# Kernel optimization log

Hardware: AMD Instinct MI355X
Metric: run time of the kernel (lower is better)

Reference implementation:

```python
import jax, jax.numpy as jnp
import numpy as np

H, C = 8, 32          # heads, per-head channels (h_feats)
NEG_SLOPE = 0.2


def setup_inputs() -> dict:
    key = jax.random.key(0)
    ks = jax.random.split(key, 9)
    N, E, F_IN, F_E = 50000, 800000, 128, 16
    x = jax.random.normal(ks[0], (N, F_IN), jnp.float32)
    edge_index = jax.random.randint(ks[1], (2, E), 0, N, jnp.int64)
    edge_attr = jax.random.normal(ks[2], (E, F_E), jnp.float32)
    s = 1.0 / np.sqrt(F_IN)
    W = jax.random.normal(ks[3], (H * C, F_IN), jnp.float32) * s
    W_edge = jax.random.normal(ks[4], (H * C, F_E), jnp.float32) * (1.0 / np.sqrt(F_E))
    att_src = jax.random.normal(ks[5], (H, C), jnp.float32) * (1.0 / np.sqrt(C))
    att_dst = jax.random.normal(ks[6], (H, C), jnp.float32) * (1.0 / np.sqrt(C))
    att_edge = jax.random.normal(ks[7], (H, C), jnp.float32) * (1.0 / np.sqrt(C))
    bias = jnp.zeros((C,), jnp.float32)
    return {"x": x, "edge_index": edge_index, "edge_attr": edge_attr,
            "W": W, "W_edge": W_edge, "att_src": att_src, "att_dst": att_dst,
            "att_edge": att_edge, "bias": bias}


def reference(x, edge_index, edge_attr, W, W_edge, att_src, att_dst, att_edge, bias):
    N = x.shape[0]
    src, dst = edge_index[0], edge_index[1]

    # --- add self loops, edge_attr fill_value='mean' (per-dst mean of incoming attrs) ---
    deg = jax.ops.segment_sum(jnp.ones_like(dst, dtype=edge_attr.dtype), dst, num_segments=N)
    loop_attr = jax.ops.segment_sum(edge_attr, dst, num_segments=N) / jnp.maximum(deg, 1.0)[:, None]
    loop = jnp.arange(N, dtype=src.dtype)
    src = jnp.concatenate([src, loop])
    dst = jnp.concatenate([dst, loop])
    ea = jnp.concatenate([edge_attr, loop_attr], axis=0)  # [E+N, F_e]

    # --- node projection and per-node attention terms ---
    xh = (x @ W.T).reshape(N, H, C)                      # [N,H,C]
    a_src = jnp.einsum('nhc,hc->nh', xh, att_src)        # [N,H]
    a_dst = jnp.einsum('nhc,hc->nh', xh, att_dst)        # [N,H]

    # edge attention folded: (lin_edge(e).view(E,H,C) * att_edge).sum(-1) == e @ M
    M = jnp.einsum('hcf,hc->fh', W_edge.reshape(H, C, -1), att_edge)  # [F_e,H]
    a_edge = ea @ M                                      # [E+N,H]

    alpha = a_src[src] + a_dst[dst] + a_edge             # [E+N,H]
    alpha = jnp.where(alpha >= 0, alpha, NEG_SLOPE * alpha)

    # --- scatter-softmax over edges grouped by dst node ---
    amax = jax.ops.segment_max(alpha, dst, num_segments=N)  # every node has a self loop
    ex = jnp.exp(alpha - amax[dst])
    denom = jax.ops.segment_sum(ex, dst, num_segments=N)
    att = ex / denom[dst]                                # [E+N,H]

    # --- weighted message scatter-sum ---
    msg = xh[src] * att[..., None]                       # [E+N,H,C]
    out = jax.ops.segment_sum(msg, dst, num_segments=N)  # [N,H,C]
    return out.mean(axis=1) + bias                       # concat=False -> head mean
```

## Files before the change

kernel.cpp:

```cpp
#include <hip/hip_runtime.h>
#include <hip/hip_fp16.h>
#include <math.h>

#define H 8
#define C 32
#define HC 256
#define FE 16
#define FIN 128
#define NEG_SLOPE 0.2f

typedef __attribute__((ext_vector_type(8))) short bf16x8;
typedef __attribute__((ext_vector_type(4))) float f32x4;

__device__ __forceinline__ unsigned short f2bf(float f) {
  unsigned int u = __float_as_uint(f);
  unsigned int lsb = (u >> 16) & 1u;
  u += 0x7fffu + lsb;
  return (unsigned short)(u >> 16);
}
__device__ __forceinline__ float bf2f(unsigned short s) {
  return __uint_as_float(((unsigned int)s) << 16);
}
__device__ __forceinline__ unsigned short f2h(float f) {
  return __half_as_ushort(__float2half(f));
}
__device__ __forceinline__ float h2f(unsigned short s) {
  return __half2float(__ushort_as_half(s));
}

__device__ __forceinline__ void split8(const float* v, bf16x8& hi, bf16x8& lo) {
#pragma unroll
  for (int i = 0; i < 8; ++i) {
    unsigned int u = __float_as_uint(v[i]);
    unsigned int hu = u & 0xffff0000u;
    float r = v[i] - __uint_as_float(hu);
    hi[i] = (short)(hu >> 16);
    lo[i] = (short)f2bf(r);
  }
}

__global__ __launch_bounds__(256) void k_xh(const float* __restrict__ x,
                                            const unsigned short* __restrict__ Whi,
                                            const unsigned short* __restrict__ Wlo,
                                            const float* __restrict__ att_src,
                                            const float* __restrict__ att_dst,
                                            unsigned short* __restrict__ xhb,
                                            float* __restrict__ a_src,
                                            float* __restrict__ a_dst,
                                            unsigned short* __restrict__ a_srch, int N) {
  int t = threadIdx.x;
  int w = t >> 6, lane = t & 63;
  int n15 = lane & 15, q = lane >> 4;
  int nodeBase = blockIdx.x * 128 + w * 32;
  int chBase = blockIdx.y * 128;

  f32x4 acc[8][2];
#pragma unroll
  for (int mt = 0; mt < 8; ++mt)
#pragma unroll
    for (int nt = 0; nt < 2; ++nt) acc[mt][nt] = (f32x4)(0.f);

  for (int ks = 0; ks < 4; ++ks) {
    int kOff = ks * 32 + q * 8;
    bf16x8 Bhi[2], Blo[2];
#pragma unroll
    for (int nt = 0; nt < 2; ++nt) {
      int node = nodeBase + nt * 16 + n15;
      int rn = (node < N) ? node : (N - 1);
      const float* px = &x[(size_t)rn * FIN + kOff];
      float vb[8];
      *(float4*)&vb[0] = *(const float4*)px;
      *(float4*)&vb[4] = *(const float4*)(px + 4);
      split8(vb, Bhi[nt], Blo[nt]);
    }
#pragma unroll
    for (int mt = 0; mt < 8; ++mt) {
      int widx = ((chBase + mt * 16 + n15) << 7) + kOff;
      bf16x8 Ahi = *(const bf16x8*)&Whi[widx];
      bf16x8 Alo = *(const bf16x8*)&Wlo[widx];
#pragma unroll
      for (int nt = 0; nt < 2; ++nt) {
        acc[mt][nt] = __builtin_amdgcn_mfma_f32_16x16x32_bf16(Ahi, Bhi[nt], acc[mt][nt], 0, 0, 0);
        acc[mt][nt] = __builtin_amdgcn_mfma_f32_16x16x32_bf16(Ahi, Blo[nt], acc[mt][nt], 0, 0, 0);
        acc[mt][nt] = __builtin_amdgcn_mfma_f32_16x16x32_bf16(Alo, Bhi[nt], acc[mt][nt], 0, 0, 0);
      }
    }
  }

  float ps[2][4] = {{0.f,0.f,0.f,0.f},{0.f,0.f,0.f,0.f}};
  float pd[2][4] = {{0.f,0.f,0.f,0.f},{0.f,0.f,0.f,0.f}};
#pragma unroll
  for (int mt = 0; mt < 8; ++mt) {
    int hl = mt >> 1;
#pragma unroll
    for (int r = 0; r < 4; ++r) {
      int ch = chBase + mt * 16 + q * 4 + r;
      float as_c = att_src[ch], ad_c = att_dst[ch];
#pragma unroll
      for (int nt = 0; nt < 2; ++nt) {
        float val = acc[mt][nt][r];
        ps[nt][hl] = fmaf(val, as_c, ps[nt][hl]);
        pd[nt][hl] = fmaf(val, ad_c, pd[nt][hl]);
      }
    }
#pragma unroll
    for (int nt = 0; nt < 2; ++nt) {
      int node = nodeBase + nt * 16 + n15;
      if (node < N) {
        ushort4 us;
        us.x = f2bf(acc[mt][nt][0]); us.y = f2bf(acc[mt][nt][1]);
        us.z = f2bf(acc[mt][nt][2]); us.w = f2bf(acc[mt][nt][3]);
        *(ushort4*)&xhb[(size_t)node * HC + chBase + mt * 16 + q * 4] = us;
      }
    }
  }
#pragma unroll
  for (int nt = 0; nt < 2; ++nt)
#pragma unroll
    for (int hl = 0; hl < 4; ++hl) {
      ps[nt][hl] += __shfl_xor(ps[nt][hl], 16, 64);
      ps[nt][hl] += __shfl_xor(ps[nt][hl], 32, 64);
      pd[nt][hl] += __shfl_xor(pd[nt][hl], 16, 64);
      pd[nt][hl] += __shfl_xor(pd[nt][hl], 32, 64);
    }
  if (q == 0) {
#pragma unroll
    for (int nt = 0; nt < 2; ++nt) {
      int node = nodeBase + nt * 16 + n15;
      if (node < N) {
        *(float4*)&a_src[node * H + blockIdx.y * 4] = make_float4(ps[nt][0], ps[nt][1], ps[nt][2], ps[nt][3]);
        *(float4*)&a_dst[node * H + blockIdx.y * 4] = make_float4(pd[nt][0], pd[nt][1], pd[nt][2], pd[nt][3]);
        unsigned int p0 = (unsigned int)f2h(ps[nt][0]) | ((unsigned int)f2h(ps[nt][1]) << 16);
        unsigned int p1 = (unsigned int)f2h(ps[nt][2]) | ((unsigned int)f2h(ps[nt][3]) << 16);
        *(uint2*)&a_srch[(size_t)node * H + blockIdx.y * 4] = make_uint2(p0, p1);
      }
    }
  }
}

__global__ __launch_bounds__(256) void k_deg(const int* __restrict__ ei,
                                             int* __restrict__ deg,
                                             int* __restrict__ rank,
                                             const float* __restrict__ W,
                                             unsigned short* __restrict__ Whi,
                                             unsigned short* __restrict__ Wlo, int E) {
  int e = blockIdx.x * 256 + threadIdx.x;
  if (e < HC * FIN) {
    float v = W[e];
    unsigned int u = __float_as_uint(v);
    unsigned int hu = u & 0xffff0000u;
    Whi[e] = (unsigned short)(hu >> 16);
    Wlo[e] = f2bf(v - __uint_as_float(hu));
  }
  if (e < E) rank[e] = atomicAdd(&deg[ei[E + e]], 1);
}

__global__ __launch_bounds__(256) void k_scan1(const int* __restrict__ deg,
                                               int* __restrict__ bsum, int N) {
  int t = threadIdx.x;
  int i = blockIdx.x * 256 + t;
  int v = (i < N) ? deg[i] : 0;
#pragma unroll
  for (int m = 1; m < 64; m <<= 1) v += __shfl_xor(v, m, 64);
  __shared__ int wsum[4];
  if ((t & 63) == 0) wsum[t >> 6] = v;
  __syncthreads();
  if (t == 0) bsum[blockIdx.x] = wsum[0] + wsum[1] + wsum[2] + wsum[3];
}

__global__ __launch_bounds__(256) void k_scan23(const int* __restrict__ deg,
                                                const int* __restrict__ bsum,
                                                int* __restrict__ rowptr, int N, int E, int nb) {
  __shared__ int sb[256];
  __shared__ int buf[256];
  int t = threadIdx.x;
  sb[t] = (t < nb) ? bsum[t] : 0;
  int i = blockIdx.x * 256 + t;
  int v = (i < N) ? deg[i] : 0;
  buf[t] = v;
  __syncthreads();
  for (int off = 1; off < 256; off <<= 1) {
    int y1 = (t >= off) ? sb[t - off] : 0;
    int y2 = (t >= off) ? buf[t - off] : 0;
    __syncthreads();
    sb[t] += y1;
    buf[t] += y2;
    __syncthreads();
  }
  int bofs = (blockIdx.x == 0) ? 0 : sb[blockIdx.x - 1];
  if (i < N) rowptr[i] = bofs + buf[t] - v;
  if (i == 0) rowptr[N] = E;
}

__global__ __launch_bounds__(256) void k_edge_scatter(const int* __restrict__ ei,
                                                      const float* __restrict__ ea,
                                                      const float* __restrict__ W_edge,
                                                      const float* __restrict__ att_edge,
                                                      const unsigned short* __restrict__ a_srch,
                                                      const int* __restrict__ rowptr,
                                                      const int* __restrict__ rank,
                                                      unsigned int* __restrict__ recs,
                                                      int* __restrict__ sarr, int E) {
  __shared__ float Ms[FE * H];
  int t = threadIdx.x;
  if (t < FE * H) {
    int f = t >> 3, h = t & 7;
    float acc = 0.f;
#pragma unroll
    for (int c = 0; c < C; ++c)
      acc += W_edge[(h * C + c) * FE + f] * att_edge[h * C + c];
    Ms[f * H + h] = acc;
  }
  __syncthreads();
  int e0 = blockIdx.x * 512 + t;
  int e1 = e0 + 256;
  bool va = (e0 < E), vb = (e1 < E);
  int ca = va ? e0 : 0, cb = vb ? e1 : 0;
  int s0 = ei[ca], d0 = ei[E + ca];
  int s1 = ei[cb], d1 = ei[E + cb];
  const float4* pA = (const float4*)&ea[(size_t)ca * FE];
  const float4* pB = (const float4*)&ea[(size_t)cb * FE];
  float4 A0 = pA[0], A1 = pA[1], A2 = pA[2], A3 = pA[3];
  float4 B0 = pB[0], B1 = pB[1], B2 = pB[2], B3 = pB[3];
  int rk0 = rank[ca], rk1 = rank[cb];
  int rp0 = rowptr[d0], rp1 = rowptr[d1];
  uint4 asA = *(const uint4*)&a_srch[(size_t)s0 * H];
  uint4 asB = *(const uint4*)&a_srch[(size_t)s1 * H];

  float eavA[FE] = {A0.x, A0.y, A0.z, A0.w, A1.x, A1.y, A1.z, A1.w,
                    A2.x, A2.y, A2.z, A2.w, A3.x, A3.y, A3.z, A3.w};
  float eavB[FE] = {B0.x, B0.y, B0.z, B0.w, B1.x, B1.y, B1.z, B1.w,
                    B2.x, B2.y, B2.z, B2.w, B3.x, B3.y, B3.z, B3.w};
  float oA[H], oB[H];
#pragma unroll
  for (int h = 0; h < H; ++h) {
    float aa = 0.f, ab = 0.f;
#pragma unroll
    for (int f = 0; f < FE; ++f) {
      float m = Ms[f * H + h];
      aa += eavA[f] * m;
      ab += eavB[f] * m;
    }
    oA[h] = aa; oB[h] = ab;
  }
  unsigned int asw[2][4] = {{asA.x, asA.y, asA.z, asA.w}, {asB.x, asB.y, asB.z, asB.w}};
  if (va) {
    int pos = rp0 + rk0;
    unsigned int rec[H];
#pragma unroll
    for (int h = 0; h < H; ++h) {
      float asv = h2f((unsigned short)((h & 1) ? (asw[0][h >> 1] >> 16) : (asw[0][h >> 1] & 0xffffu)));
      rec[h] = (unsigned int)f2h(oA[h] + asv) | ((unsigned int)f2h(oA[h]) << 16);
    }
    uint4* rp = (uint4*)&recs[(size_t)pos * 8];
    rp[0] = make_uint4(rec[0], rec[1], rec[2], rec[3]);
    rp[1] = make_uint4(rec[4], rec[5], rec[6], rec[7]);
    sarr[pos] = s0;
  }
  if (vb) {
    int pos = rp1 + rk1;
    unsigned int rec[H];
#pragma unroll
    for (int h = 0; h < H; ++h) {
      float asv = h2f((unsigned short)((h & 1) ? (asw[1][h >> 1] >> 16) : (asw[1][h >> 1] & 0xffffu)));
      rec[h] = (unsigned int)f2h(oB[h] + asv) | ((unsigned int)f2h(oB[h]) << 16);
    }
    uint4* rp = (uint4*)&recs[(size_t)pos * 8];
    rp[0] = make_uint4(rec[0], rec[1], rec[2], rec[3]);
    rp[1] = make_uint4(rec[4], rec[5], rec[6], rec[7]);
    sarr[pos] = s1;
  }
}

__global__ __launch_bounds__(256) void k_node(const unsigned short* __restrict__ xhb,
                                              const float* __restrict__ a_src,
                                              const float* __restrict__ a_dst,
                                              const unsigned int* __restrict__ recs,
                                              const int* __restrict__ sarr,
                                              const int* __restrict__ rowptr,
                                              const float* __restrict__ bias,
                                              float* __restrict__ out, int N) {
  __shared__ float wlds[4][512];
  __shared__ int   slds[4][64];
  int wv = threadIdx.x >> 6;
  int lane = threadIdx.x & 63;
  int n = blockIdx.x * 4 + wv;
  if (n >= N) return;
  int start = rowptr[n];
  int deg = rowptr[n + 1] - start;
  int jmax = (deg < 64) ? deg : 64;
  int nit = (jmax + 7) >> 3;
  int padded = nit << 3;
  int h = lane & 7, esub = lane >> 3;
  float adst = a_dst[n * H + h];
  float asrc = a_src[n * H + h];

  if (lane < padded) slds[wv][lane] = (lane < jmax) ? sarr[start + lane] : n;

  const unsigned int* rb = recs + (size_t)start * 8 + lane;
  unsigned int u[8] = {0, 0, 0, 0, 0, 0, 0, 0};
#pragma unroll
  for (int it = 0; it < 8; ++it)
    if (it < nit) u[it] = rb[it * 64];

  float den = 0.f, psum = 0.f;
#pragma unroll
  for (int it = 0; it < 8; ++it)
    if (it < nit) {
      int j = it * 8 + esub;
      bool val = (j < jmax);
      float raw = h2f((unsigned short)(u[it] >> 16));
      float a = h2f((unsigned short)(u[it] & 0xffffu)) + adst;
      a = fmaxf(a, NEG_SLOPE * a);
      float w = val ? __expf(a) : 0.f;
      psum += val ? raw : 0.f;
      den += w;
      wlds[wv][it * 64 + lane] = w;
    }
  for (int j0 = 64; j0 < deg; j0 += 8) {
    int j = j0 + esub;
    if (j < deg) {
      unsigned int t = recs[(size_t)(start + j) * 8 + h];
      psum += h2f((unsigned short)(t >> 16));
      float a = h2f((unsigned short)(t & 0xffffu)) + adst;
      a = fmaxf(a, NEG_SLOPE * a);
      den += __expf(a);
    }
  }
#pragma unroll
  for (int m = 8; m <= 32; m <<= 1) {
    den += __shfl_xor(den, m, 64);
    psum += __shfl_xor(psum, m, 64);
  }
  float aself = asrc + adst + psum / fmaxf((float)deg, 1.f);
  aself = fmaxf(aself, NEG_SLOPE * aself);
  float wself = __expf(aself);
  float inv = 1.f / (den + wself);

  int hc = lane >> 3;
  float inv_c  = __shfl(inv, hc, 64);
  float ws_c   = __shfl(wself, hc, 64);
  float adst_c = __shfl(adst, hc, 64);
  float accx, accy, accz, accw;
  {
    uint2 su = ((const uint2*)(xhb + (((size_t)n) << 8)))[lane];
    accx = ws_c * __uint_as_float(su.x << 16);
    accy = ws_c * __uint_as_float(su.x & 0xffff0000u);
    accz = ws_c * __uint_as_float(su.y << 16);
    accw = ws_c * __uint_as_float(su.y & 0xffff0000u);
  }
  uint2 v0[8]; float w0[8];
  if (padded > 0) {
#pragma unroll
    for (int k = 0; k < 8; ++k) {
      w0[k] = wlds[wv][k * 8 + hc];
      v0[k] = ((const uint2*)(xhb + (((size_t)slds[wv][k]) << 8)))[lane];
    }
  }
  for (int j0 = 0; j0 < padded; j0 += 8) {
    uint2 v1[8]; float w1[8];
    int jn = j0 + 8;
    if (jn < padded) {
#pragma unroll
      for (int k = 0; k < 8; ++k) {
        w1[k] = wlds[wv][(jn + k) * 8 + hc];
        v1[k] = ((const uint2*)(xhb + (((size_t)slds[wv][jn + k]) << 8)))[lane];
      }
    }
#pragma unroll
    for (int k = 0; k < 8; ++k) {
      accx = fmaf(__uint_as_float(v0[k].x << 16), w0[k], accx);
      accy = fmaf(__uint_as_float(v0[k].x & 0xffff0000u), w0[k], accy);
      accz = fmaf(__uint_as_float(v0[k].y << 16), w0[k], accz);
      accw = fmaf(__uint_as_float(v0[k].y & 0xffff0000u), w0[k], accw);
    }
#pragma unroll
    for (int k = 0; k < 8; ++k) { v0[k] = v1[k]; w0[k] = w1[k]; }
  }
  for (int j = 64; j < deg; ++j) {
    unsigned int t = recs[(size_t)(start + j) * 8 + hc];
    int src = sarr[start + j];
    float a = h2f((unsigned short)(t & 0xffffu)) + adst_c;
    a = fmaxf(a, NEG_SLOPE * a);
    float wj = __expf(a);
    uint2 v = ((const uint2*)(xhb + (((size_t)src) << 8)))[lane];
    accx = fmaf(__uint_as_float(v.x << 16), wj, accx);
    accy = fmaf(__uint_as_float(v.x & 0xffff0000u), wj, accy);
    accz = fmaf(__uint_as_float(v.y << 16), wj, accz);
    accw = fmaf(__uint_as_float(v.y & 0xffff0000u), wj, accw);
  }
  accx *= inv_c; accy *= inv_c; accz *= inv_c; accw *= inv_c;

#pragma unroll
  for (int m = 8; m <= 32; m <<= 1) {
    accx += __shfl_xor(accx, m, 64);
    accy += __shfl_xor(accy, m, 64);
    accz += __shfl_xor(accz, m, 64);
    accw += __shfl_xor(accw, m, 64);
  }
  if (lane < 8) {
    float4 b = ((const float4*)bias)[lane];
    float4 o;
    o.x = accx * 0.125f + b.x;
    o.y = accy * 0.125f + b.y;
    o.z = accz * 0.125f + b.z;
    o.w = accw * 0.125f + b.w;
    ((float4*)&out[(size_t)n * C])[lane] = o;
  }
}

extern "C" void kernel_launch(void* const* d_in, const int* in_sizes, int n_in,
                              void* d_out, int out_size, void* d_ws, size_t ws_size,
                              hipStream_t stream) {
  const float* x        = (const float*)d_in[0];
  const int*   ei       = (const int*)d_in[1];
  const float* ea       = (const float*)d_in[2];
  const float* W        = (const float*)d_in[3];
  const float* W_edge   = (const float*)d_in[4];
  const float* att_src  = (const float*)d_in[5];
  const float* att_dst  = (const float*)d_in[6];
  const float* att_edge = (const float*)d_in[7];
  const float* bias     = (const float*)d_in[8];
  float* out = (float*)d_out;

  int N = in_sizes[0] / FIN;
  int E = in_sizes[1] / 2;
  int nb = (N + 255) / 256;

  char* ws = (char*)d_ws;
  auto take = [&](size_t bytes) {
    char* p = ws;
    ws += (bytes + 255) & ~(size_t)255;
    return p;
  };
  unsigned short* xhb    = (unsigned short*)take((size_t)N * HC * 2);
  float*          a_src  = (float*)take((size_t)N * H * 4);
  float*          a_dst  = (float*)take((size_t)N * H * 4);
  unsigned short* a_srch = (unsigned short*)take((size_t)N * H * 2);
  unsigned int*   recs   = (unsigned int*)take((size_t)E * 32);
  int*            sarr   = (int*)take((size_t)E * 4);
  unsigned short* Whi    = (unsigned short*)take((size_t)HC * FIN * 2);
  unsigned short* Wlo    = (unsigned short*)take((size_t)HC * FIN * 2);
  int*            deg    = (int*)take((size_t)N * 4);
  int*            rowptr = (int*)take((size_t)(N + 1) * 4);
  int*            rank   = (int*)take((size_t)E * 4);
  int*            bsum   = (int*)take((size_t)nb * 4);

  hipMemsetAsync(deg, 0, (size_t)N * 4, stream);
  k_deg<<<(E + 255) / 256, 256, 0, stream>>>(ei, deg, rank, W, Whi, Wlo, E);
  k_xh<<<dim3((N + 127) / 128, 2), 256, 0, stream>>>(x, Whi, Wlo, att_src, att_dst, xhb, a_src, a_dst, a_srch, N);
  k_scan1<<<nb, 256, 0, stream>>>(deg, bsum, N);
  k_scan23<<<nb, 256, 0, stream>>>(deg, bsum, rowptr, N, E, nb);
  k_edge_scatter<<<(E + 511) / 512, 256, 0, stream>>>(ei, ea, W_edge, att_edge, a_srch, rowptr, rank, recs, sarr, E);
  k_node<<<(N + 3) / 4, 256, 0, stream>>>(xhb, a_src, a_dst, recs, sarr, rowptr, bias, out, N);
}
```

Measured before the change: 303.4 us.

## Merge scan kernels with decoupled lookback, use packed FMA, drop fp32 a_src

Replaces the two-kernel degree scan with one kernel that uses decoupled lookback over an atomic status array, saving a launch. The status array is zeroed by the same memset as deg. The node kernel now reads the fp16 a_src copy instead of a separate fp32 buffer, which drops that buffer and its writes. The gather loop uses v_pk_fma_f32 on pairs of edges with a reordered LDS weight layout, and its register double-buffer prefetch is removed. Risks are the lower-precision a_src, spin-waiting that depends on blocks being scheduled in order, and reduced latency hiding in the gather loop.

```diff
diff --git a/kernel.cpp b/kernel.cpp
--- a/kernel.cpp
+++ b/kernel.cpp
@@ -11,6 +11,7 @@
 
 typedef __attribute__((ext_vector_type(8))) short bf16x8;
 typedef __attribute__((ext_vector_type(4))) float f32x4;
+typedef __attribute__((ext_vector_type(2))) float f32x2;
 
 __device__ __forceinline__ unsigned short f2bf(float f) {
   unsigned int u = __float_as_uint(f);
@@ -26,6 +27,9 @@
 }
 __device__ __forceinline__ float h2f(unsigned short s) {
   return __half2float(__ushort_as_half(s));
+}
+__device__ __forceinline__ void pkfma(f32x2& acc, f32x2 x, f32x2 w) {
+  asm volatile("v_pk_fma_f32 %0, %1, %2, %0" : "+v"(acc) : "v"(x), "v"(w));
 }
 
 __device__ __forceinline__ void split8(const float* v, bf16x8& hi, bf16x8& lo) {
@@ -45,7 +49,6 @@
                                             const float* __restrict__ att_src,
                                             const float* __restrict__ att_dst,
                                             unsigned short* __restrict__ xhb,
-                                            float* __restrict__ a_src,
                                             float* __restrict__ a_dst,
                                             unsigned short* __restrict__ a_srch, int N) {
   int t = threadIdx.x;
@@ -128,7 +131,6 @@
     for (int nt = 0; nt < 2; ++nt) {
       int node = nodeBase + nt * 16 + n15;
       if (node < N) {
-        *(float4*)&a_src[node * H + blockIdx.y * 4] = make_float4(ps[nt][0], ps[nt][1], ps[nt][2], ps[nt][3]);
         *(float4*)&a_dst[node * H + blockIdx.y * 4] = make_float4(pd[nt][0], pd[nt][1], pd[nt][2], pd[nt][3]);
         unsigned int p0 = (unsigned int)f2h(ps[nt][0]) | ((unsigned int)f2h(ps[nt][1]) << 16);
         unsigned int p1 = (unsigned int)f2h(ps[nt][2]) | ((unsigned int)f2h(ps[nt][3]) << 16);
@@ -155,40 +157,45 @@
   if (e < E) rank[e] = atomicAdd(&deg[ei[E + e]], 1);
 }
 
-__global__ __launch_bounds__(256) void k_scan1(const int* __restrict__ deg,
-                                               int* __restrict__ bsum, int N) {
-  int t = threadIdx.x;
-  int i = blockIdx.x * 256 + t;
-  int v = (i < N) ? deg[i] : 0;
-#pragma unroll
-  for (int m = 1; m < 64; m <<= 1) v += __shfl_xor(v, m, 64);
-  __shared__ int wsum[4];
-  if ((t & 63) == 0) wsum[t >> 6] = v;
-  __syncthreads();
-  if (t == 0) bsum[blockIdx.x] = wsum[0] + wsum[1] + wsum[2] + wsum[3];
-}
-
-__global__ __launch_bounds__(256) void k_scan23(const int* __restrict__ deg,
-                                                const int* __restrict__ bsum,
-                                                int* __restrict__ rowptr, int N, int E, int nb) {
-  __shared__ int sb[256];
+__global__ __launch_bounds__(256) void k_scan(const int* __restrict__ deg,
+                                              unsigned long long* __restrict__ st,
+                                              int* __restrict__ rowptr, int N, int E) {
   __shared__ int buf[256];
-  int t = threadIdx.x;
-  sb[t] = (t < nb) ? bsum[t] : 0;
-  int i = blockIdx.x * 256 + t;
+  __shared__ int bofs_sh;
+  int t = threadIdx.x, b = blockIdx.x;
+  int i = b * 256 + t;
   int v = (i < N) ? deg[i] : 0;
   buf[t] = v;
   __syncthreads();
   for (int off = 1; off < 256; off <<= 1) {
-    int y1 = (t >= off) ? sb[t - off] : 0;
-    int y2 = (t >= off) ? buf[t - off] : 0;
+    int y = (t >= off) ? buf[t - off] : 0;
     __syncthreads();
-    sb[t] += y1;
-    buf[t] += y2;
+    buf[t] += y;
     __syncthreads();
   }
-  int bofs = (blockIdx.x == 0) ? 0 : sb[blockIdx.x - 1];
-  if (i < N) rowptr[i] = bofs + buf[t] - v;
+  if (t == 0) {
+    int agg = buf[255];
+    if (b == 0) {
+      __hip_atomic_store(&st[0], (2ull << 32) | (unsigned int)agg, __ATOMIC_RELEASE, __HIP_MEMORY_SCOPE_AGENT);
+      bofs_sh = 0;
+    } else {
+      __hip_atomic_store(&st[b], (1ull << 32) | (unsigned int)agg, __ATOMIC_RELEASE, __HIP_MEMORY_SCOPE_AGENT);
+      int excl = 0;
+      int p = b - 1;
+      while (true) {
+        unsigned long long s = __hip_atomic_load(&st[p], __ATOMIC_ACQUIRE, __HIP_MEMORY_SCOPE_AGENT);
+        unsigned int flag = (unsigned int)(s >> 32);
+        if (flag == 0u) { __builtin_amdgcn_s_sleep(1); continue; }
+        excl += (int)(unsigned int)(s & 0xffffffffull);
+        if (flag == 2u) break;
+        --p;
+      }
+      __hip_atomic_store(&st[b], (2ull << 32) | (unsigned int)(excl + agg), __ATOMIC_RELEASE, __HIP_MEMORY_SCOPE_AGENT);
+      bofs_sh = excl;
+    }
+  }
+  __syncthreads();
+  if (i < N) rowptr[i] = bofs_sh + buf[t] - v;
   if (i == 0) rowptr[N] = E;
 }
 
@@ -273,7 +280,7 @@
 }
 
 __global__ __launch_bounds__(256) void k_node(const unsigned short* __restrict__ xhb,
-                                              const float* __restrict__ a_src,
+                                              const unsigned short* __restrict__ a_srch,
                                               const float* __restrict__ a_dst,
                                               const unsigned int* __restrict__ recs,
                                               const int* __restrict__ sarr,
@@ -293,7 +300,7 @@
   int padded = nit << 3;
   int h = lane & 7, esub = lane >> 3;
   float adst = a_dst[n * H + h];
-  float asrc = a_src[n * H + h];
+  float asrc = h2f(a_srch[(size_t)n * H + h]);
 
   if (lane < padded) slds[wv][lane] = (lane < jmax) ? sarr[start + lane] : n;
 
@@ -301,8 +308,12 @@
   unsigned int u[8] = {0, 0, 0, 0, 0, 0, 0, 0};
 #pragma unroll
   for (int it = 0; it < 8; ++it)
-    if (it < nit) u[it] = rb[it * 64];
-
+    if (it < nit) {
+      int j = it * 8 + esub;
+      if (j < jmax) u[it] = rb[it * 64];
+    }
+
+  int widx = ((esub >> 1) << 4) + (h << 1) + (esub & 1);
   float den = 0.f, psum = 0.f;
 #pragma unroll
   for (int it = 0; it < 8; ++it)
@@ -315,14 +326,14 @@
       float w = val ? __expf(a) : 0.f;
       psum += val ? raw : 0.f;
       den += w;
-      wlds[wv][it * 64 + lane] = w;
+      wlds[wv][it * 64 + widx] = w;
     }
   for (int j0 = 64; j0 < deg; j0 += 8) {
     int j = j0 + esub;
     if (j < deg) {
-      unsigned int t = recs[(size_t)(start + j) * 8 + h];
-      psum += h2f((unsigned short)(t >> 16));
-      float a = h2f((unsigned short)(t & 0xffffu)) + adst;
+      unsigned int t2 = recs[(size_t)(start + j) * 8 + h];
+      psum += h2f((unsigned short)(t2 >> 16));
+      float a = h2f((unsigned short)(t2 & 0xffffu)) + adst;
       a = fmaxf(a, NEG_SLOPE * a);
       den += __expf(a);
     }
@@ -341,46 +352,42 @@
   float inv_c  = __shfl(inv, hc, 64);
   float ws_c   = __shfl(wself, hc, 64);
   float adst_c = __shfl(adst, hc, 64);
-  float accx, accy, accz, accw;
+  f32x2 A0, A1, A2, A3;
   {
     uint2 su = ((const uint2*)(xhb + (((size_t)n) << 8)))[lane];
-    accx = ws_c * __uint_as_float(su.x << 16);
-    accy = ws_c * __uint_as_float(su.x & 0xffff0000u);
-    accz = ws_c * __uint_as_float(su.y << 16);
-    accw = ws_c * __uint_as_float(su.y & 0xffff0000u);
-  }
-  uint2 v0[8]; float w0[8];
-  if (padded > 0) {
-#pragma unroll
-    for (int k = 0; k < 8; ++k) {
-      w0[k] = wlds[wv][k * 8 + hc];
-      v0[k] = ((const uint2*)(xhb + (((size_t)slds[wv][k]) << 8)))[lane];
-    }
+    A0[0] = ws_c * __uint_as_float(su.x << 16);         A0[1] = 0.f;
+    A1[0] = ws_c * __uint_as_float(su.x & 0xffff0000u); A1[1] = 0.f;
+    A2[0] = ws_c * __uint_as_float(su.y << 16);         A2[1] = 0.f;
+    A3[0] = ws_c * __uint_as_float(su.y & 0xffff0000u); A3[1] = 0.f;
   }
   for (int j0 = 0; j0 < padded; j0 += 8) {
-    uint2 v1[8]; float w1[8];
-    int jn = j0 + 8;
-    if (jn < padded) {
-#pragma unroll
-      for (int k = 0; k < 8; ++k) {
-        w1[k] = wlds[wv][(jn + k) * 8 + hc];
-        v1[k] = ((const uint2*)(xhb + (((size_t)slds[wv][jn + k]) << 8)))[lane];
-      }
-    }
-#pragma unroll
-    for (int k = 0; k < 8; ++k) {
-      accx = fmaf(__uint_as_float(v0[k].x << 16), w0[k], accx);
-      accy = fmaf(__uint_as_float(v0[k].x & 0xffff0000u), w0[k], accy);
-      accz = fmaf(__uint_as_float(v0[k].y << 16), w0[k], accz);
-      accw = fmaf(__uint_as_float(v0[k].y & 0xffff0000u), w0[k], accw);
-    }
-#pragma unroll
-    for (int k = 0; k < 8; ++k) { v0[k] = v1[k]; w0[k] = w1[k]; }
-  }
+    uint2 v[8];
+#pragma unroll
+    for (int k = 0; k < 8; ++k)
+      v[k] = ((const uint2*)(xhb + (((size_t)slds[wv][j0 + k]) << 8)))[lane];
+#pragma unroll
+    for (int k2 = 0; k2 < 4; ++k2) {
+      f32x2 wp = *(const f32x2*)&wlds[wv][j0 * 8 + k2 * 16 + hc * 2];
+      uint2 va = v[2 * k2], vb2 = v[2 * k2 + 1];
+      f32x2 p;
+      p[0] = __uint_as_float(va.x << 16);          p[1] = __uint_as_float(vb2.x << 16);
+      pkfma(A0, p, wp);
+      p[0] = __uint_as_float(va.x & 0xffff0000u);  p[1] = __uint_as_float(vb2.x & 0xffff0000u);
+      pkfma(A1, p, wp);
+      p[0] = __uint_as_float(va.y << 16);          p[1] = __uint_as_float(vb2.y << 16);
+      pkfma(A2, p, wp);
+      p[0] = __uint_as_float(va.y & 0xffff0000u);  p[1] = __uint_as_float(vb2.y & 0xffff0000u);
+      pkfma(A3, p, wp);
+    }
+  }
+  float accx = A0[0] + A0[1];
+  float accy = A1[0] + A1[1];
+  float accz = A2[0] + A2[1];
+  float accw = A3[0] + A3[1];
   for (int j = 64; j < deg; ++j) {
-    unsigned int t = recs[(size_t)(start + j) * 8 + hc];
     int src = sarr[start + j];
-    float a = h2f((unsigned short)(t & 0xffffu)) + adst_c;
+    unsigned int t2 = recs[(size_t)(start + j) * 8 + hc];
+    float a = h2f((unsigned short)(t2 & 0xffffu)) + adst_c;
     a = fmaxf(a, NEG_SLOPE * a);
     float wj = __expf(a);
     uint2 v = ((const uint2*)(xhb + (((size_t)src) << 8)))[lane];
@@ -434,23 +441,23 @@
     return p;
   };
   unsigned short* xhb    = (unsigned short*)take((size_t)N * HC * 2);
-  float*          a_src  = (float*)take((size_t)N * H * 4);
   float*          a_dst  = (float*)take((size_t)N * H * 4);
   unsigned short* a_srch = (unsigned short*)take((size_t)N * H * 2);
   unsigned int*   recs   = (unsigned int*)take((size_t)E * 32);
   int*            sarr   = (int*)take((size_t)E * 4);
   unsigned short* Whi    = (unsigned short*)take((size_t)HC * FIN * 2);
   unsigned short* Wlo    = (unsigned short*)take((size_t)HC * FIN * 2);
-  int*            deg    = (int*)take((size_t)N * 4);
+  size_t degBytes = ((size_t)N * 4 + 7) & ~(size_t)7;
+  char*  zbase    = take(degBytes + (size_t)nb * 8);
+  int*            deg    = (int*)zbase;
+  unsigned long long* st = (unsigned long long*)(zbase + degBytes);
   int*            rowptr = (int*)take((size_t)(N + 1) * 4);
   int*            rank   = (int*)take((size_t)E * 4);
-  int*            bsum   = (int*)take((size_t)nb * 4);
-
-  hipMemsetAsync(deg, 0, (size_t)N * 4, stream);
+
+  hipMemsetAsync(zbase, 0, degBytes + (size_t)nb * 8, stream);
   k_deg<<<(E + 255) / 256, 256, 0, stream>>>(ei, deg, rank, W, Whi, Wlo, E);
-  k_xh<<<dim3((N + 127) / 128, 2), 256, 0, stream>>>(x, Whi, Wlo, att_src, att_dst, xhb, a_src, a_dst, a_srch, N);
-  k_scan1<<<nb, 256, 0, stream>>>(deg, bsum, N);
-  k_scan23<<<nb, 256, 0, stream>>>(deg, bsum, rowptr, N, E, nb);
+  k_xh<<<dim3((N + 127) / 128, 2), 256, 0, stream>>>(x, Whi, Wlo, att_src, att_dst, xhb, a_dst, a_srch, N);
+  k_scan<<<nb, 256, 0, stream>>>(deg, st, rowptr, N, E);
   k_edge_scatter<<<(E + 511) / 512, 256, 0, stream>>>(ei, ea, W_edge, att_edge, a_srch, rowptr, rank, recs, sarr, E);
-  k_node<<<(N + 3) / 4, 256, 0, stream>>>(xhb, a_src, a_dst, recs, sarr, rowptr, bias, out, N);
-}
+  k_node<<<(N + 3) / 4, 256, 0, stream>>>(xhb, a_srch, a_dst, recs, sarr, rowptr, bias, out, N);
+}
```

New measurement: 330.8 us. +9.0%, slower.
